# Kernel optimization log

Measured on AMD Instinct MI355X. Metric: run time of the kernel, lower is better.

## Reference

```python
import jax, jax.numpy as jnp
import numpy as np

IN_DIM, OUT_DIM = 1024, 1024
GRID_SIZE, K = 8, 3
TOKENS = 8192


def b_splines(x, grid, k):
    # x: [B, in_dim], grid: [in_dim, grid_size + 2k + 1]
    x = x[..., None]  # [B, in_dim, 1]
    # order-0 indicator bases: [B, in_dim, grid_size + 2k]
    bases = ((x >= grid[:, :-1]) & (x < grid[:, 1:])).astype(x.dtype)
    # Cox-de Boor recursion up to order k -> [B, in_dim, grid_size + k]
    for kk in range(1, k + 1):
        left = (x - grid[:, : -(kk + 1)]) / (grid[:, kk:-1] - grid[:, : -(kk + 1)])
        right = (grid[:, kk + 1:] - x) / (grid[:, kk + 1:] - grid[:, 1:-kk])
        bases = left * bases[..., :-1] + right * bases[..., 1:]
    return bases


def setup_inputs() -> dict:
    key = jax.random.key(0)
    k1, k2, k3 = jax.random.split(key, 3)
    x = jax.random.normal(k1, (TOKENS, IN_DIM), dtype=jnp.float32)
    # grid buffer: arange(-k, grid_size+k+1) * step + grid_range[0], repeated per in_dim
    grid_range = (-1.0, 1.0)
    step = (grid_range[1] - grid_range[0]) / GRID_SIZE
    grid_row = np.arange(-K, GRID_SIZE + K + 1, dtype=np.float32) * step + grid_range[0]
    grid = jnp.asarray(np.tile(grid_row, (IN_DIM, 1)))  # [in_dim, 15]
    coeff = jax.random.normal(k2, (OUT_DIM, IN_DIM, GRID_SIZE + K), dtype=jnp.float32) * 0.1
    scale_base = 1.0 / np.sqrt(IN_DIM) + jax.random.normal(k3, (OUT_DIM, IN_DIM), dtype=jnp.float32) * 0.1
    scale_spline = jnp.ones((1,), dtype=jnp.float32)
    return {"x": x, "grid": grid, "coeff": coeff, "scale_base": scale_base,
            "scale_spline": scale_spline}


def reference(x, grid, coeff, scale_base, scale_spline):
    splines = b_splines(x, grid, K)                      # [B, in, G+K]
    y_b = jnp.matmul(jax.nn.silu(x), scale_base.T)       # [B, out]
    w = coeff * scale_spline                             # scalar broadcast [out, in, G+K]
    y_spline = jnp.einsum('big,oig->bo', splines, w)     # [B, out]
    return y_b + y_spline
```

## Files before the change

kernel.cpp:

```cpp
#include <hip/hip_runtime.h>
#include <hip/hip_bf16.h>
#include <stdint.h>

typedef __attribute__((ext_vector_type(8))) short short8;
typedef __attribute__((ext_vector_type(16))) float floatx16;
typedef unsigned short u16;

#define IN_DIM  1024
#define OUT_DIM 1024
#define NG      11
#define GK      12
#define KDIM    (IN_DIM * GK)
#define TOKENS  8192

#define GBK     64
#define G2R     9
#define G2OPS   36
#define ABUF    (256 * 72)

#define FBK     48
#define FROW    56
#define FBUF    (256 * FROW)
#define FOPS    4

__device__ __forceinline__ u16 f2bf(float f) {
  uint32_t u = __float_as_uint(f);
  uint32_t r = (u + 0x7fffu + ((u >> 16) & 1u)) >> 16;
  return (u16)r;
}

__device__ __forceinline__ void expand_regs(float x, float g0, float inv_h,
                                            uint64_t& V0, uint64_t& V1, uint64_t& V2)
{
  float t  = (x - g0) * inv_h;
  float fc = floorf(t);
  int   c  = (int)fc;
  float u  = t - fc;
  float u2 = u * u;
  float w1 = 1.0f - u;
  float b0 = (w1 * w1 * w1) * (1.0f / 6.0f);
  float b1 = (0.5f * u - 1.0f) * u2 + (2.0f / 3.0f);
  float b2 = ((-0.5f * u + 0.5f) * u + 0.5f) * u + (1.0f / 6.0f);
  float b3 = (u2 * u) * (1.0f / 6.0f);
  float sil = x / (1.0f + __expf(-x));

  uint64_t P = (uint64_t)f2bf(b0) | ((uint64_t)f2bf(b1) << 16)
             | ((uint64_t)f2bf(b2) << 32) | ((uint64_t)f2bf(b3) << 48);
  int  k  = c - 3;
  bool cv = (c >= 0) && (c <= 13);
  int  kneg = (k < 0) ? -k : 0;
  uint64_t Pc = cv ? (P >> (16 * kneg)) : 0ull;
  uint32_t sh = (uint32_t)(16 * ((k < 0) ? 0 : k));

  V0 = (sh < 64)  ? (Pc << (sh & 63)) : 0ull;
  V1 = (sh == 0)  ? 0ull :
       (sh < 64)  ? (Pc >> ((64 - sh) & 63)) :
       (sh < 128) ? (Pc << ((sh - 64) & 63)) : 0ull;
  V2 = (sh <= 64) ? 0ull :
       (sh < 128) ? (Pc >> ((128 - sh) & 63)) :
                    (Pc << ((sh - 128) & 63));
  V2 = (V2 & 0x0000FFFFFFFFFFFFull) | ((uint64_t)f2bf(sil) << 48);
}

__device__ __forceinline__ void async16(const u16* g, u16* l) {
  __builtin_amdgcn_global_load_lds(
      (const __attribute__((address_space(1))) uint32_t*)g,
      (__attribute__((address_space(3))) uint32_t*)l,
      16, 0, 0);
}

__global__ __launch_bounds__(256) void prep_kernel(
    const float* __restrict__ coeff, const float* __restrict__ sb,
    const float* __restrict__ ss_p, u16* __restrict__ Wt,
    const float* __restrict__ X, const float* __restrict__ grid,
    u16* __restrict__ Aexp)
{
  __shared__ __align__(16) char smem_c[49152];
  const int tid = threadIdx.x;

  if (blockIdx.x < 4096) {
    float* cf = (float*)smem_c;
    u16*   st = (u16*)(smem_c + 11264);
    const int b   = blockIdx.x;
    const int o   = b >> 2;
    const int i0  = (b & 3) * 256;
    const float* cbase = coeff + (size_t)o * (IN_DIM * NG) + (size_t)i0 * NG;
#pragma unroll
    for (int p = 0; p < NG; ++p) cf[p * 256 + tid] = cbase[p * 256 + tid];
    const float ss  = ss_p[0];
    const float sbv = sb[(size_t)o * IN_DIM + i0 + tid];
    __syncthreads();
    const float* cp = cf + tid * NG;
    u16 h[GK];
#pragma unroll
    for (int g = 0; g < NG; ++g) h[g] = f2bf(cp[g] * ss);
    h[NG] = f2bf(sbv);
    uint64_t V0 = (uint64_t)h[0] | ((uint64_t)h[1] << 16) | ((uint64_t)h[2] << 32) | ((uint64_t)h[3] << 48);
    uint64_t V1 = (uint64_t)h[4] | ((uint64_t)h[5] << 16) | ((uint64_t)h[6] << 32) | ((uint64_t)h[7] << 48);
    uint64_t V2 = (uint64_t)h[8] | ((uint64_t)h[9] << 16) | ((uint64_t)h[10] << 32) | ((uint64_t)h[11] << 48);
    uint64_t* sp = (uint64_t*)(st + tid * GK);
    sp[0] = V0; sp[1] = V1; sp[2] = V2;
    __syncthreads();
    const uint4* src = (const uint4*)st;
    uint4* dst = (uint4*)(Wt + (size_t)b * (256 * GK));
    dst[tid] = src[tid];
    if (tid < 128) dst[256 + tid] = src[256 + tid];
  } else {
    uint4 (*st4)[1536] = (uint4 (*)[1536])smem_c;
    const float g0    = grid[0];
    const float inv_h = 1.0f / (grid[1] - grid[0]);
    const int bb   = blockIdx.x - 4096;
    const int row0 = bb * 8;

    uint64_t ev[12];
    {
      float4 xv = *(const float4*)(X + (size_t)row0 * IN_DIM + tid * 4);
      expand_regs(xv.x, g0, inv_h, ev[0], ev[1], ev[2]);
      expand_regs(xv.y, g0, inv_h, ev[3], ev[4], ev[5]);
      expand_regs(xv.z, g0, inv_h, ev[6], ev[7], ev[8]);
      expand_regs(xv.w, g0, inv_h, ev[9], ev[10], ev[11]);
#pragma unroll
      for (int j = 0; j < 6; ++j) {
        uint4 w;
        w.x = (uint32_t)ev[2*j];     w.y = (uint32_t)(ev[2*j] >> 32);
        w.z = (uint32_t)ev[2*j+1];   w.w = (uint32_t)(ev[2*j+1] >> 32);
        st4[0][tid * 6 + j] = w;
      }
    }
    __syncthreads();

    for (int rr = 0; rr < 8; ++rr) {
      const int p = rr & 1;
      uint4 v[6];
#pragma unroll
      for (int j = 0; j < 6; ++j) v[j] = st4[p][j * 256 + tid];
      if (rr + 1 < 8) {
        float4 xv = *(const float4*)(X + (size_t)(row0 + rr + 1) * IN_DIM + tid * 4);
        expand_regs(xv.x, g0, inv_h, ev[0], ev[1], ev[2]);
        expand_regs(xv.y, g0, inv_h, ev[3], ev[4], ev[5]);
        expand_regs(xv.z, g0, inv_h, ev[6], ev[7], ev[8]);
        expand_regs(xv.w, g0, inv_h, ev[9], ev[10], ev[11]);
      }
      uint4* dst = (uint4*)(Aexp + (size_t)(row0 + rr) * KDIM);
#pragma unroll
      for (int j = 0; j < 6; ++j) dst[j * 256 + tid] = v[j];
      if (rr + 1 < 8) {
#pragma unroll
        for (int j = 0; j < 6; ++j) {
          uint4 w;
          w.x = (uint32_t)ev[2*j];     w.y = (uint32_t)(ev[2*j] >> 32);
          w.z = (uint32_t)ev[2*j+1];   w.w = (uint32_t)(ev[2*j+1] >> 32);
          st4[p ^ 1][tid * 6 + j] = w;
        }
      }
      __syncthreads();
    }
  }
}

__global__ __launch_bounds__(512, 2) void gemm_pre_kernel(
    const u16* __restrict__ A, const u16* __restrict__ Wt,
    float* __restrict__ out, float* __restrict__ part, int k_iters)
{
  __shared__ __align__(16) u16 S[4 * ABUF];

  const int tid  = threadIdx.x;
  const int lane = tid & 63;
  const int wave = tid >> 6;
  const int s    = blockIdx.x >> 7;
  const int r    = blockIdx.x & 127;
  const int bm   = r & 31;
  const int bn   = r >> 5;
  const int wm   = (wave >> 2) * 128;
  const int wn   = (wave & 3) * 64;
  const int l31  = lane & 31;
  const int g8   = lane >> 5;

  floatx16 acc[4][2];
#pragma unroll
  for (int a = 0; a < 4; ++a)
#pragma unroll
    for (int b = 0; b < 2; ++b)
#pragma unroll
      for (int rr = 0; rr < 16; ++rr) acc[a][b][rr] = 0.f;

  const size_t k0 = (size_t)s * k_iters * GBK;
  const u16* src[9]; int dof[9];
#pragma unroll
  for (int j = 0; j < 9; ++j) {
    int q    = wave + 8 * j;
    bool isA = (q < 36);
    int oq   = isA ? q : q - 36;
    int gidx  = oq * 64 + lane;
    int row   = gidx / 9;
    int chunk = gidx - row * 9;
    int c8    = (chunk == 8) ? 0 : chunk;
    src[j] = (isA ? A + (size_t)(bm * 256 + row) * KDIM
                  : Wt + (size_t)(bn * 256 + row) * KDIM) + k0 + c8 * 8;
    dof[j] = (isA ? 0 : 2 * ABUF) + oq * 512;
  }

  const int NT = k_iters;

#pragma unroll
  for (int j = 0; j < 9; ++j) async16(src[j], S + dof[j]);
  asm volatile("s_waitcnt vmcnt(0)" ::: "memory");
  __builtin_amdgcn_s_barrier();
  __builtin_amdgcn_sched_barrier(0);
#pragma unroll
  for (int j = 0; j < 9; ++j) async16(src[j] + GBK, S + ABUF + dof[j]);

  for (int t = 0; t < NT; ++t) {
    const u16* Ab = S + (t & 1) * ABUF;
    const u16* Bb = S + 2 * ABUF + (t & 1) * ABUF;

    __builtin_amdgcn_s_setprio(1);
#pragma unroll
    for (int ks = 0; ks < 4; ++ks) {
      short8 bf0 = *(const short8*)&Bb[(wn +      l31) * 72 + (2 * ks + g8) * 8];
      short8 bf1 = *(const short8*)&Bb[(wn + 32 + l31) * 72 + (2 * ks + g8) * 8];
#pragma unroll
      for (int m = 0; m < 4; ++m) {
        short8 af = *(const short8*)&Ab[(wm + m * 32 + l31) * 72 + (2 * ks + g8) * 8];
        acc[m][0] = __builtin_amdgcn_mfma_f32_32x32x16_bf16(af, bf0, acc[m][0], 0, 0, 0);
        acc[m][1] = __builtin_amdgcn_mfma_f32_32x32x16_bf16(af, bf1, acc[m][1], 0, 0, 0);
      }
    }
    __builtin_amdgcn_s_setprio(0);

    __builtin_amdgcn_s_barrier();
    __builtin_amdgcn_sched_barrier(0);
    if (t + 2 < NT) {
      u16* D = S + (t & 1) * ABUF;
      const size_t ko = (size_t)(t + 2) * GBK;
#pragma unroll
      for (int j = 0; j < 9; ++j) async16(src[j] + ko, D + dof[j]);
      asm volatile("s_waitcnt vmcnt(9)" ::: "memory");
    } else {
      asm volatile("s_waitcnt vmcnt(0)" ::: "memory");
    }
    __builtin_amdgcn_s_barrier();
    __builtin_amdgcn_sched_barrier(0);
  }

  float* op = (s == 0) ? out : part;
#pragma unroll
  for (int m = 0; m < 4; ++m)
#pragma unroll
    for (int n = 0; n < 2; ++n) {
      const int row0 = bm * 256 + wm + m * 32 + 4 * g8;
      const int col  = bn * 256 + wn + n * 32 + l31;
#pragma unroll
      for (int reg = 0; reg < 16; ++reg) {
        int row = row0 + (reg & 3) + 8 * (reg >> 2);
        op[(size_t)row * OUT_DIM + col] = acc[m][n][reg];
      }
    }
}

__global__ __launch_bounds__(256) void reduce_kernel(
    float* __restrict__ out, const float* __restrict__ part)
{
  size_t i = (size_t)blockIdx.x * 256 + threadIdx.x;
  float4* o = (float4*)out;
  const float4* p = (const float4*)part;
  float4 a = o[i], b = p[i];
  a.x += b.x; a.y += b.y; a.z += b.z; a.w += b.w;
  o[i] = a;
}

__device__ __forceinline__ void expand2(float2 xv, float g0, float inv_h, uint64_t e[6]) {
  expand_regs(xv.x, g0, inv_h, e[0], e[1], e[2]);
  expand_regs(xv.y, g0, inv_h, e[3], e[4], e[5]);
}
__device__ __forceinline__ void write_ev(u16* abase, int awoff, const uint64_t e[6]) {
  uint4* w = (uint4*)(abase + awoff);
  uint4 w0, w1, w2;
  w0.x = (uint32_t)e[0]; w0.y = (uint32_t)(e[0] >> 32);
  w0.z = (uint32_t)e[1]; w0.w = (uint32_t)(e[1] >> 32);
  w1.x = (uint32_t)e[2]; w1.y = (uint32_t)(e[2] >> 32);
  w1.z = (uint32_t)e[3]; w1.w = (uint32_t)(e[3] >> 32);
  w2.x = (uint32_t)e[4]; w2.y = (uint32_t)(e[4] >> 32);
  w2.z = (uint32_t)e[5]; w2.w = (uint32_t)(e[5] >> 32);
  w[0] = w0; w[1] = w1; w[2] = w2;
}

__global__ __launch_bounds__(256) void pack_wt_kernel(
    const float* __restrict__ coeff, const float* __restrict__ sb,
    const float* __restrict__ ss_p, u16* __restrict__ Wt)
{
  __shared__ float cf[256 * NG];
  __shared__ __align__(16) u16 st[256 * GK];
  const int tid = threadIdx.x;
  const int b   = blockIdx.x;
  const int o   = b >> 2;
  const int i0  = (b & 3) * 256;
  const float* cbase = coeff + (size_t)o * (IN_DIM * NG) + (size_t)i0 * NG;
#pragma unroll
  for (int p = 0; p < NG; ++p) cf[p * 256 + tid] = cbase[p * 256 + tid];
  const float ss  = ss_p[0];
  const float sbv = sb[(size_t)o * IN_DIM + i0 + tid];
  __syncthreads();
  const float* cp = cf + tid * NG;
  u16 h[GK];
#pragma unroll
  for (int g = 0; g < NG; ++g) h[g] = f2bf(cp[g] * ss);
  h[NG] = f2bf(sbv);
  uint64_t V0 = (uint64_t)h[0] | ((uint64_t)h[1] << 16) | ((uint64_t)h[2] << 32) | ((uint64_t)h[3] << 48);
  uint64_t V1 = (uint64_t)h[4] | ((uint64_t)h[5] << 16) | ((uint64_t)h[6] << 32) | ((uint64_t)h[7] << 48);
  uint64_t V2 = (uint64_t)h[8] | ((uint64_t)h[9] << 16) | ((uint64_t)h[10] << 32) | ((uint64_t)h[11] << 48);
  uint64_t* sp = (uint64_t*)(st + tid * GK);
  sp[0] = V0; sp[1] = V1; sp[2] = V2;
  __syncthreads();
  const uint4* src = (const uint4*)st;
  uint4* dst = (uint4*)(Wt + (size_t)b * (256 * GK));
  dst[tid] = src[tid];
  if (tid < 128) dst[256 + tid] = src[256 + tid];
}

__global__ __launch_bounds__(512, 2) void gemm_fused2_kernel(
    const float* __restrict__ X, const float* __restrict__ grid,
    const u16* __restrict__ Wt, float* __restrict__ out, float* __restrict__ part,
    int k_iters)
{
  __shared__ __align__(16) u16 S[4 * FBUF];

  const int tid  = threadIdx.x;
  const int lane = tid & 63;
  const int wave = tid >> 6;
  const int s    = blockIdx.x >> 7;
  const int r    = blockIdx.x & 127;
  const int bm   = r & 31;
  const int bn   = r >> 5;
  const int wm   = (wave >> 2) * 128;
  const int wn   = (wave & 3) * 64;
  const int l31  = lane & 31;
  const int g8   = lane >> 5;

  const float g0    = grid[0];
  const float inv_h = 1.0f / (grid[1] - grid[0]);

  floatx16 acc[4][2];
#pragma unroll
  for (int a = 0; a < 4; ++a)
#pragma unroll
    for (int b = 0; b < 2; ++b)
#pragma unroll
      for (int rr = 0; rr < 16; ++rr) acc[a][b][rr] = 0.f;

  const int kb = s * k_iters * FBK;
  const u16* bsrc[FOPS]; int bdof[FOPS];
#pragma unroll
  for (int j = 0; j < FOPS; ++j) {
    int o  = wave + 8 * j;
    int oc = (o < 28) ? o : 27;
    int gidx = oc * 64 + lane;
    int row  = gidx / 7;
    int sl   = gidx - row * 7;
    int c6   = (sl == 6) ? 0 : sl;
    bsrc[j] = Wt + (size_t)(bn * 256 + row) * KDIM + kb + c6 * 8;
    bdof[j] = oc * 512;
  }

  const int arow  = tid >> 1;
  const int cp    = (tid & 1) * 2;
  const float* xp = X + (size_t)(bm * 256 + arow) * IN_DIM + s * (k_iters * 4) + cp;
  const int awoff = arow * FROW + cp * 12;

  const int NT = k_iters;

  float2 x0    = *(const float2*)(xp + 0);
  float2 x1    = *(const float2*)(xp + 4);
  float2 x_use = *(const float2*)(xp + 8);
  float2 x_mid = *(const float2*)(xp + 12);
  float2 x_new = x_use;

#pragma unroll
  for (int j = 0; j < FOPS; ++j) async16(bsrc[j],       S + 2 * FBUF + bdof[j]);
#pragma unroll
  for (int j = 0; j < FOPS; ++j) async16(bsrc[j] + FBK, S + 3 * FBUF + bdof[j]);
  {
    uint64_t e[6];
    expand2(x0, g0, inv_h, e); write_ev(S, awoff, e);
    expand2(x1, g0, inv_h, e); write_ev(S + FBUF, awoff, e);
  }
  asm volatile("s_waitcnt vmcnt(0) lgkmcnt(0)" ::: "memory");
  __builtin_amdgcn_s_barrier();
  __builtin_amdgcn_sched_barrier(0);

  for (int t = 0; t < NT; ++t) {
    const int p = t & 1;
    const u16* Ab = S + p * FBUF;
    const u16* Bb = S + 2 * FBUF + p * FBUF;

    uint64_t e[6];
    const bool dostage = (t + 2 < NT);
    if (dostage) expand2(x_use, g0, inv_h, e);

    __builtin_amdgcn_s_setprio(1);
#pragma unroll
    for (int ks = 0; ks < 3; ++ks) {
      const int cc = (2 * ks + g8) * 8;
      short8 bf0 = *(const short8*)&Bb[(wn +      l31) * FROW + cc];
      short8 bf1 = *(const short8*)&Bb[(wn + 32 + l31) * FROW + cc];
#pragma unroll
      for (int m = 0; m < 4; ++m) {
        short8 af = *(const short8*)&Ab[(wm + m * 32 + l31) * FROW + cc];
        acc[m][0] = __builtin_amdgcn_mfma_f32_32x32x16_bf16(af, bf0, acc[m][0], 0, 0, 0);
        acc[m][1] = __builtin_amdgcn_mfma_f32_32x32x16_bf16(af, bf1, acc[m][1], 0, 0, 0);
      }
    }
    __builtin_amdgcn_s_setprio(0);

    __builtin_amdgcn_s_barrier();
    __builtin_amdgcn_sched_barrier(0);

    if (dostage) {
      const int ko = (t + 2) * FBK;
      u16* Bd = S + 2 * FBUF + p * FBUF;
#pragma unroll
      for (int j = 0; j < FOPS; ++j) async16(bsrc[j] + ko, Bd + bdof[j]);
      write_ev(S + p * FBUF, awoff, e);
      if (t + 4 < NT) {
        x_new = *(const float2*)(xp + (size_t)(t + 4) * 4);
        asm volatile("s_waitcnt vmcnt(5) lgkmcnt(0)" ::: "memory");
      } else {
        asm volatile("s_waitcnt vmcnt(4) lgkmcnt(0)" ::: "memory");
      }
    } else {
      asm volatile("s_waitcnt vmcnt(0) lgkmcnt(0)" ::: "memory");
    }
    __builtin_amdgcn_s_barrier();
    __builtin_amdgcn_sched_barrier(0);

    x_use = x_mid; x_mid = x_new;
  }

  float* op = (s == 0) ? out : part;
#pragma unroll
  for (int m = 0; m < 4; ++m)
#pragma unroll
    for (int n = 0; n < 2; ++n) {
      const int row0 = bm * 256 + wm + m * 32 + 4 * g8;
      const int col  = bn * 256 + wn + n * 32 + l31;
#pragma unroll
      for (int reg = 0; reg < 16; ++reg) {
        int row = row0 + (reg & 3) + 8 * (reg >> 2);
        op[(size_t)row * OUT_DIM + col] = acc[m][n][reg];
      }
    }
}

extern "C" void kernel_launch(void* const* d_in, const int* in_sizes, int n_in,
                              void* d_out, int out_size, void* d_ws, size_t ws_size,
                              hipStream_t stream) {
  const float* x     = (const float*)d_in[0];
  const float* grid  = (const float*)d_in[1];
  const float* coeff = (const float*)d_in[2];
  const float* sb    = (const float*)d_in[3];
  const float* ss    = (const float*)d_in[4];
  float* out = (float*)d_out;

  u16* Wt = (u16*)d_ws;
  const size_t wt_bytes   = (size_t)OUT_DIM * KDIM * 2;
  const size_t aexp_bytes = (size_t)TOKENS * KDIM * 2;
  const size_t part_bytes = (size_t)TOKENS * OUT_DIM * 4;

  if (ws_size >= wt_bytes + aexp_bytes + part_bytes) {
    u16*   Aexp = (u16*)((char*)d_ws + wt_bytes);
    float* part = (float*)((char*)d_ws + wt_bytes + aexp_bytes);
    prep_kernel<<<4096 + TOKENS / 8, 256, 0, stream>>>(coeff, sb, ss, Wt, x, grid, Aexp);
    gemm_pre_kernel<<<128 * 2, 512, 0, stream>>>(Aexp, Wt, out, part, 96);
    reduce_kernel<<<(TOKENS * OUT_DIM / 4) / 256, 256, 0, stream>>>(out, part);
  } else if (ws_size >= wt_bytes + part_bytes) {
    float* part = (float*)((char*)d_ws + wt_bytes);
    pack_wt_kernel<<<(OUT_DIM * IN_DIM) / 256, 256, 0, stream>>>(coeff, sb, ss, Wt);
    gemm_fused2_kernel<<<128 * 2, 512, 0, stream>>>(x, grid, Wt, out, part, 128);
    reduce_kernel<<<(TOKENS * OUT_DIM / 4) / 256, 256, 0, stream>>>(out, part);
  } else {
    pack_wt_kernel<<<(OUT_DIM * IN_DIM) / 256, 256, 0, stream>>>(coeff, sb, ss, Wt);
    gemm_fused2_kernel<<<128, 512, 0, stream>>>(x, grid, Wt, out, nullptr, 256);
  }
}
```

Before: 368.1 us.

## Interleave next-tile async loads with per-k-slice MFMA in single-lookahead pipeline

Restructures the GEMM main loop from a prefetch-two-ahead double buffer, with bulk loads issued after the compute, into a one-ahead scheme. The next tile's global-to-LDS loads are split into three groups, each issued during one of the first three k-slices, with barriers around every k-slice. All A fragments are loaded before each MFMA burst, and the wait for global loads happens only at the end of the tile. This aims to spread memory issue across compute and cut the idle time of the bulk load phase. In exchange it adds more barriers per tile, and the shorter prefetch distance may expose global latency.

```diff
diff --git a/kernel.cpp b/kernel.cpp
--- a/kernel.cpp
+++ b/kernel.cpp
@@ -207,40 +207,52 @@
   asm volatile("s_waitcnt vmcnt(0)" ::: "memory");
   __builtin_amdgcn_s_barrier();
   __builtin_amdgcn_sched_barrier(0);
-#pragma unroll
-  for (int j = 0; j < 9; ++j) async16(src[j] + GBK, S + ABUF + dof[j]);
 
   for (int t = 0; t < NT; ++t) {
-    const u16* Ab = S + (t & 1) * ABUF;
-    const u16* Bb = S + 2 * ABUF + (t & 1) * ABUF;
-
-    __builtin_amdgcn_s_setprio(1);
+    const int p = t & 1;
+    const u16* Ab = S + p * ABUF;
+    const u16* Bb = S + 2 * ABUF + p * ABUF;
+    const bool st = (t + 1 < NT);
+    const size_t ko = (size_t)(t + 1) * GBK;
+    u16* Dbase = S + (p ^ 1) * ABUF;
+
 #pragma unroll
     for (int ks = 0; ks < 4; ++ks) {
       short8 bf0 = *(const short8*)&Bb[(wn +      l31) * 72 + (2 * ks + g8) * 8];
       short8 bf1 = *(const short8*)&Bb[(wn + 32 + l31) * 72 + (2 * ks + g8) * 8];
-#pragma unroll
-      for (int m = 0; m < 4; ++m) {
-        short8 af = *(const short8*)&Ab[(wm + m * 32 + l31) * 72 + (2 * ks + g8) * 8];
-        acc[m][0] = __builtin_amdgcn_mfma_f32_32x32x16_bf16(af, bf0, acc[m][0], 0, 0, 0);
-        acc[m][1] = __builtin_amdgcn_mfma_f32_32x32x16_bf16(af, bf1, acc[m][1], 0, 0, 0);
-      }
-    }
-    __builtin_amdgcn_s_setprio(0);
-
-    __builtin_amdgcn_s_barrier();
-    __builtin_amdgcn_sched_barrier(0);
-    if (t + 2 < NT) {
-      u16* D = S + (t & 1) * ABUF;
-      const size_t ko = (size_t)(t + 2) * GBK;
-#pragma unroll
-      for (int j = 0; j < 9; ++j) async16(src[j] + ko, D + dof[j]);
-      asm volatile("s_waitcnt vmcnt(9)" ::: "memory");
-    } else {
-      asm volatile("s_waitcnt vmcnt(0)" ::: "memory");
-    }
-    __builtin_amdgcn_s_barrier();
-    __builtin_amdgcn_sched_barrier(0);
+      short8 af0 = *(const short8*)&Ab[(wm +       l31) * 72 + (2 * ks + g8) * 8];
+      short8 af1 = *(const short8*)&Ab[(wm +  32 + l31) * 72 + (2 * ks + g8) * 8];
+      short8 af2 = *(const short8*)&Ab[(wm +  64 + l31) * 72 + (2 * ks + g8) * 8];
+      short8 af3 = *(const short8*)&Ab[(wm +  96 + l31) * 72 + (2 * ks + g8) * 8];
+      if (st && ks < 3) {
+#pragma unroll
+        for (int jj = 0; jj < 3; ++jj) {
+          const int j = ks * 3 + jj;
+          async16(src[j] + ko, Dbase + dof[j]);
+        }
+      }
+      __builtin_amdgcn_sched_barrier(0);
+      __builtin_amdgcn_s_barrier();
+      asm volatile("s_waitcnt lgkmcnt(0)" ::: "memory");
+      __builtin_amdgcn_sched_barrier(0);
+
+      __builtin_amdgcn_s_setprio(1);
+      acc[0][0] = __builtin_amdgcn_mfma_f32_32x32x16_bf16(af0, bf0, acc[0][0], 0, 0, 0);
+      acc[0][1] = __builtin_amdgcn_mfma_f32_32x32x16_bf16(af0, bf1, acc[0][1], 0, 0, 0);
+      acc[1][0] = __builtin_amdgcn_mfma_f32_32x32x16_bf16(af1, bf0, acc[1][0], 0, 0, 0);
+      acc[1][1] = __builtin_amdgcn_mfma_f32_32x32x16_bf16(af1, bf1, acc[1][1], 0, 0, 0);
+      acc[2][0] = __builtin_amdgcn_mfma_f32_32x32x16_bf16(af2, bf0, acc[2][0], 0, 0, 0);
+      acc[2][1] = __builtin_amdgcn_mfma_f32_32x32x16_bf16(af2, bf1, acc[2][1], 0, 0, 0);
+      acc[3][0] = __builtin_amdgcn_mfma_f32_32x32x16_bf16(af3, bf0, acc[3][0], 0, 0, 0);
+      acc[3][1] = __builtin_amdgcn_mfma_f32_32x32x16_bf16(af3, bf1, acc[3][1], 0, 0, 0);
+      __builtin_amdgcn_s_setprio(0);
+
+      if (ks == 3 && st) {
+        asm volatile("s_waitcnt vmcnt(0)" ::: "memory");
+      }
+      __builtin_amdgcn_sched_barrier(0);
+      __builtin_amdgcn_s_barrier();
+    }
   }
 
   float* op = (s == 0) ? out : part;
```

After: 385.3 us. +4.7%, slower.
